# Performance work log

Measured on AMD Instinct MI355X. Metric: run time of the kernel, lower is better.

## Reference

```python
import jax, jax.numpy as jnp
import numpy as np

NUM_HEADS = 16
ROPE_BASE = 10000.0


def _rope_cos_sin(seq_len, head_dim, dtype):
    # freqs for the half-dim; original caches cat(freqs, freqs) and then applies
    # the rotation per-half, which is equivalent to using the half-size tables.
    inv_freq = 1.0 / (ROPE_BASE ** (jnp.arange(0, head_dim, 2, dtype=jnp.float32) / head_dim))
    t = jnp.arange(seq_len, dtype=jnp.float32)
    freqs = jnp.einsum('i,j->ij', t, inv_freq)  # [S, hd/2]
    return jnp.cos(freqs).astype(dtype), jnp.sin(freqs).astype(dtype)


def _apply_rotary(x, cos, sin):
    # x: [B, H, S, hd]; cos/sin: [S, hd/2] broadcast over B, H
    half = x.shape[-1] // 2
    x1, x2 = x[..., :half], x[..., half:]
    return jnp.concatenate([x1 * cos - x2 * sin, x2 * cos + x1 * sin], axis=-1)


def setup_inputs() -> dict:
    key = jax.random.key(0)
    ks = jax.random.split(key, 5)
    D = 2048
    B, S = 2, 2048
    std = 1.0 / np.sqrt(D)
    return {
        'x': jax.random.normal(ks[0], (B, S, D), dtype=jnp.float32),
        'Wq': jax.random.normal(ks[1], (D, D), dtype=jnp.float32) * std,
        'Wk': jax.random.normal(ks[2], (D, D), dtype=jnp.float32) * std,
        'Wv': jax.random.normal(ks[3], (D, D), dtype=jnp.float32) * std,
        'Wo': jax.random.normal(ks[4], (D, D), dtype=jnp.float32) * std,
    }


def reference(x, Wq, Wk, Wv, Wo):
    B, S, D = x.shape
    H = NUM_HEADS
    hd = D // H
    scale = hd ** -0.5

    def proj(W):  # torch Linear: y = x @ W.T -> [B, H, S, hd]
        return (x @ W.T).reshape(B, S, H, hd).transpose(0, 2, 1, 3)

    q, k, v = proj(Wq), proj(Wk), proj(Wv)

    cos, sin = _rope_cos_sin(S, hd, x.dtype)
    q = _apply_rotary(q, cos, sin)
    k = _apply_rotary(k, cos, sin)

    scores = jnp.einsum('bhqd,bhkd->bhqk', q, k) * scale  # full O(S^2) scores
    attn = jax.nn.softmax(scores, axis=-1)
    out = jnp.einsum('bhqk,bhkd->bhqd', attn, v)
    out = out.transpose(0, 2, 1, 3).reshape(B, S, D)
    return out @ Wo.T
```

## Files before the change

kernel.cpp:

```cpp
#include <hip/hip_runtime.h>
#include <cstdint>

typedef __attribute__((ext_vector_type(8))) short bf16x8;
typedef __attribute__((ext_vector_type(4))) float f32x4;
typedef __attribute__((ext_vector_type(16))) float f32x16;

__device__ inline unsigned short f2bf(float f) {
  uint32_t u = __float_as_uint(f);
  uint32_t lsb = (u >> 16) & 1u;
  u += 0x7fffu + lsb;
  return (unsigned short)(u >> 16);
}
__device__ inline float bf2f(unsigned short b) {
  return __uint_as_float(((uint32_t)b) << 16);
}
__device__ inline uint32_t cvt_pk_bf16(float lo, float hi) {
  uint32_t r;
  asm volatile("v_cvt_pk_bf16_f32 %0, %1, %2" : "=v"(r) : "v"(lo), "v"(hi));
  return r;
}

#define GLOAD16(gp, lp)                                                        \
  __builtin_amdgcn_global_load_lds(                                            \
      (const __attribute__((address_space(1))) void*)(gp),                     \
      (__attribute__((address_space(3))) void*)(lp), 16, 0, 0)

__global__ void cvt_f32_bf16(const float* __restrict__ in,
                             unsigned short* __restrict__ out, int n) {
  int i = (blockIdx.x * 256 + threadIdx.x) * 4;
  if (i >= n) return;
  float4 v = *(const float4*)(in + i);
  unsigned short o[4] = {f2bf(v.x), f2bf(v.y), f2bf(v.z), f2bf(v.w)};
  *(uint64_t*)(out + i) = *(const uint64_t*)o;
}

__global__ void rope_table_k(float* __restrict__ ctab, float* __restrict__ stab) {
  int i = blockIdx.x * 256 + threadIdx.x;
  int s = i >> 6, j = i & 63;
  float invf = expf(-(float)j * (9.210340371976184f / 64.0f));
  float ang = (float)s * invf;
  ctab[i] = cosf(ang);
  stab[i] = sinf(ang);
}

__global__ void rope_apply_k(unsigned short* __restrict__ qb,
                             unsigned short* __restrict__ kb,
                             const float* __restrict__ ctab,
                             const float* __restrict__ stab) {
  int row = blockIdx.x * 4 + (threadIdx.x >> 6);
  int t = threadIdx.x & 63;
  int s = row & 2047;
  int bh = (row >> 11) & 31;
  int isK = row >> 16;
  unsigned short* base = isK ? kb : qb;
  float qs = isK ? 1.0f : (0.08838834764831845f * 1.4426950408889634f);
  unsigned short* p = base + ((size_t)bh * 2048 + s) * 128;
  float c = ctab[s * 64 + t], sn = stab[s * 64 + t];
  float x1 = bf2f(p[t]), x2 = bf2f(p[t + 64]);
  p[t] = f2bf((x1 * c - x2 * sn) * qs);
  p[t + 64] = f2bf((x2 * c + x1 * sn) * qs);
}

__global__ void transpose_v_k(const unsigned short* __restrict__ v,
                              unsigned short* __restrict__ vt) {
  __shared__ unsigned short tile[64][72];
  int bh = blockIdx.x, st = blockIdx.y, dt = blockIdx.z;
  const unsigned short* src = v + ((size_t)bh * 2048 + st * 64) * 128 + dt * 64;
  unsigned short* dst = vt + ((size_t)bh * 128 + dt * 64) * 2048 + st * 64;
  int t = threadIdx.x;
  int r = t >> 2, c0 = (t & 3) * 16;
  *(bf16x8*)&tile[r][c0] = *(const bf16x8*)(src + (size_t)r * 128 + c0);
  *(bf16x8*)&tile[r][c0 + 8] = *(const bf16x8*)(src + (size_t)r * 128 + c0 + 8);
  __syncthreads();
  unsigned short o[16];
#pragma unroll
  for (int i = 0; i < 16; i++) o[i] = tile[c0 + i][r];
  *(bf16x8*)(dst + (size_t)r * 2048 + c0) = *(const bf16x8*)&o[0];
  *(bf16x8*)(dst + (size_t)r * 2048 + c0 + 8) = *(const bf16x8*)&o[8];
}

template <int EPI>
__global__ __launch_bounds__(256, 2) void gemm_bt(
    const unsigned short* __restrict__ A, const unsigned short* __restrict__ Bm,
    float* __restrict__ Cf, unsigned short* __restrict__ q_out,
    unsigned short* __restrict__ k_out, unsigned short* __restrict__ v_out,
    int M, int N, int K) {
  __shared__ unsigned short sA[128 * 32];
  __shared__ unsigned short sB[128 * 32];
  const int t = threadIdx.x;
  const int w = t >> 6, l = t & 63;
  const int wr = w >> 1, wc = w & 1;
  const int bm = blockIdx.x * 128, bn = blockIdx.y * 128;
  const int lr = l & 15, lg = l >> 4;
  f32x4 acc[4][4] = {};

  const int srow = w * 16 + (l >> 2);
  const int sseg = (l & 3) * 8;
  const unsigned short* ga = A + (size_t)(bm + srow) * K + sseg;
  const unsigned short* gb = Bm + (size_t)(bn + srow) * K + sseg;
  unsigned short* lA = sA + w * 512 + l * 8;
  unsigned short* lB = sB + w * 512 + l * 8;

  for (int kt = 0; kt < K; kt += 32) {
    __syncthreads();
    GLOAD16(ga + kt, lA);
    GLOAD16(ga + kt + (size_t)64 * K, lA + 2048);
    GLOAD16(gb + kt, lB);
    GLOAD16(gb + kt + (size_t)64 * K, lB + 2048);
    __syncthreads();
    bf16x8 af[4], bfv[4];
#pragma unroll
    for (int m = 0; m < 4; m++)
      af[m] = *(const bf16x8*)(sA + (wr * 64 + m * 16 + lr) * 32 + lg * 8);
#pragma unroll
    for (int n = 0; n < 4; n++)
      bfv[n] = *(const bf16x8*)(sB + (wc * 64 + n * 16 + lr) * 32 + lg * 8);
#pragma unroll
    for (int m = 0; m < 4; m++)
#pragma unroll
      for (int n = 0; n < 4; n++)
        acc[m][n] = __builtin_amdgcn_mfma_f32_16x16x32_bf16(af[m], bfv[n],
                                                            acc[m][n], 0, 0, 0);
  }

#pragma unroll
  for (int m = 0; m < 4; m++) {
#pragma unroll
    for (int n = 0; n < 4; n++) {
      int gm0 = bm + wr * 64 + m * 16 + lg * 4;
      int gn = bn + wc * 64 + n * 16 + lr;
#pragma unroll
      for (int j = 0; j < 4; j++) {
        float v = acc[m][n][j];
        int gm = gm0 + j;
        if (EPI == 0) {
          Cf[(size_t)gm * N + gn] = v;
        } else {
          int which = gn >> 11, rem = gn & 2047;
          int h = rem >> 7, d = rem & 127;
          int b = gm >> 11, s = gm & 2047;
          unsigned short* dst = which == 0 ? q_out : (which == 1 ? k_out : v_out);
          dst[(((size_t)(b * 16 + h)) * 2048 + s) * 128 + d] = f2bf(v);
        }
      }
    }
  }
}

template <int EPI>
__global__ __launch_bounds__(512, 1) void gemm256(
    const unsigned short* __restrict__ A, const unsigned short* __restrict__ Bm,
    float* __restrict__ Cf, unsigned short* __restrict__ q_out,
    unsigned short* __restrict__ k_out, unsigned short* __restrict__ v_out,
    int M, int N, int K, int nbm) {
  __shared__ unsigned short sA[2][2][256 * 32];
  __shared__ unsigned short sB[2][2][256 * 32];

  const int t = threadIdx.x;
  const int w = t >> 6, l = t & 63;
  const int wr = w >> 2, wc = w & 3;
  const int lr = l & 15, lg = l >> 4;
  const int gsw = (lg ^ (lr & 3)) * 8;

  const int cpx = gridDim.x >> 3;
  const int bid = blockIdx.x;
  const int swz = (bid & 7) * cpx + (bid >> 3);
  const int bm = (swz % nbm) * 256, bn = (swz / nbm) * 256;

  f32x4 acc[8][4] = {};

  int rowi[2], goff[2];
#pragma unroll
  for (int i = 0; i < 2; i++) {
    int idx = i * 512 + t;
    rowi[i] = idx >> 2;
    goff[i] = ((idx & 3) ^ (rowi[i] & 3)) * 8;
  }
  const unsigned short* Ab = A + (size_t)bm * K;
  const unsigned short* Bb = Bm + (size_t)bn * K;

#define STAGE256(Xb, plane, koff)                                              \
  do {                                                                         \
    _Pragma("unroll") for (int i = 0; i < 2; i++)                              \
        GLOAD16(Xb + (size_t)rowi[i] * K + (koff) + goff[i],                   \
                (plane) + (i * 512 + t) * 8);                                  \
  } while (0)

  STAGE256(Ab, sA[0][0], 0);
  STAGE256(Bb, sB[0][0], 0);
  STAGE256(Ab, sA[0][1], 32);
  STAGE256(Bb, sB[0][1], 32);
  asm volatile("s_waitcnt vmcnt(4)" ::: "memory");
  __builtin_amdgcn_s_barrier();

  const int NT = K >> 6;
  for (int t2 = 0; t2 < NT; ++t2) {
    const int db = t2 & 1, dn = db ^ 1;
    const int kt = (t2 + 1 < NT ? t2 + 1 : t2) * 64;
    bf16x8 a[4], a2[4], b[4];

#pragma unroll
    for (int mf = 0; mf < 4; mf++)
      a[mf] = *(const bf16x8*)&sA[db][0][(wr * 128 + mf * 16 + lr) * 32 + gsw];
#pragma unroll
    for (int nf = 0; nf < 4; nf++)
      b[nf] = *(const bf16x8*)&sB[db][0][(wc * 64 + nf * 16 + lr) * 32 + gsw];
    STAGE256(Ab, sA[dn][0], kt);
    __builtin_amdgcn_s_barrier();
    asm volatile("s_waitcnt lgkmcnt(0)" ::: "memory");
    __builtin_amdgcn_sched_barrier(0);
    __builtin_amdgcn_s_setprio(1);
#pragma unroll
    for (int mf = 0; mf < 4; mf++)
#pragma unroll
      for (int nf = 0; nf < 4; nf++)
        acc[mf][nf] = __builtin_amdgcn_mfma_f32_16x16x32_bf16(a[mf], b[nf],
                                                              acc[mf][nf], 0, 0, 0);
    __builtin_amdgcn_s_setprio(0);
    __builtin_amdgcn_s_barrier();

#pragma unroll
    for (int mf = 0; mf < 4; mf++)
      a2[mf] = *(const bf16x8*)&sA[db][0][(wr * 128 + (mf + 4) * 16 + lr) * 32 + gsw];
    STAGE256(Bb, sB[dn][0], kt);
    __builtin_amdgcn_s_barrier();
    asm volatile("s_waitcnt lgkmcnt(0)" ::: "memory");
    __builtin_amdgcn_sched_barrier(0);
    __builtin_amdgcn_s_setprio(1);
#pragma unroll
    for (int mf = 0; mf < 4; mf++)
#pragma unroll
      for (int nf = 0; nf < 4; nf++)
        acc[mf + 4][nf] = __builtin_amdgcn_mfma_f32_16x16x32_bf16(
            a2[mf], b[nf], acc[mf + 4][nf], 0, 0, 0);
    __builtin_amdgcn_s_setprio(0);
    asm volatile("s_waitcnt vmcnt(4)" ::: "memory");
    __builtin_amdgcn_s_barrier();

#pragma unroll
    for (int mf = 0; mf < 4; mf++)
      a[mf] = *(const bf16x8*)&sA[db][1][(wr * 128 + mf * 16 + lr) * 32 + gsw];
#pragma unroll
    for (int nf = 0; nf < 4; nf++)
      b[nf] = *(const bf16x8*)&sB[db][1][(wc * 64 + nf * 16 + lr) * 32 + gsw];
    STAGE256(Ab, sA[dn][1], kt + 32);
    __builtin_amdgcn_s_barrier();
    asm volatile("s_waitcnt lgkmcnt(0)" ::: "memory");
    __builtin_amdgcn_sched_barrier(0);
    __builtin_amdgcn_s_setprio(1);
#pragma unroll
    for (int mf = 0; mf < 4; mf++)
#pragma unroll
      for (int nf = 0; nf < 4; nf++)
        acc[mf][nf] = __builtin_amdgcn_mfma_f32_16x16x32_bf16(a[mf], b[nf],
                                                              acc[mf][nf], 0, 0, 0);
    __builtin_amdgcn_s_setprio(0);
    __builtin_amdgcn_s_barrier();

#pragma unroll
    for (int mf = 0; mf < 4; mf++)
      a2[mf] = *(const bf16x8*)&sA[db][1][(wr * 128 + (mf + 4) * 16 + lr) * 32 + gsw];
    STAGE256(Bb, sB[dn][1], kt + 32);
    __builtin_amdgcn_s_barrier();
    asm volatile("s_waitcnt lgkmcnt(0)" ::: "memory");
    __builtin_amdgcn_sched_barrier(0);
    __builtin_amdgcn_s_setprio(1);
#pragma unroll
    for (int mf = 0; mf < 4; mf++)
#pragma unroll
      for (int nf = 0; nf < 4; nf++)
        acc[mf + 4][nf] = __builtin_amdgcn_mfma_f32_16x16x32_bf16(
            a2[mf], b[nf], acc[mf + 4][nf], 0, 0, 0);
    __builtin_amdgcn_s_setprio(0);
    asm volatile("s_waitcnt vmcnt(4)" ::: "memory");
    __builtin_amdgcn_s_barrier();
  }

#pragma unroll
  for (int mf = 0; mf < 8; mf++) {
#pragma unroll
    for (int nf = 0; nf < 4; nf++) {
      int gm0 = bm + wr * 128 + mf * 16 + lg * 4;
      int gn = bn + wc * 64 + nf * 16 + lr;
#pragma unroll
      for (int j = 0; j < 4; j++) {
        float v = acc[mf][nf][j];
        int gm = gm0 + j;
        if (EPI == 0) {
          Cf[(size_t)gm * N + gn] = v;
        } else {
          int which = gn >> 11, rem = gn & 2047;
          int h = rem >> 7, d = rem & 127;
          int b = gm >> 11, s = gm & 2047;
          unsigned short* dst = which == 0 ? q_out : (which == 1 ? k_out : v_out);
          dst[(((size_t)(b * 16 + h)) * 2048 + s) * 128 + d] = f2bf(v);
        }
      }
    }
  }
}

__global__ __launch_bounds__(256, 2) void attn_k(
    const unsigned short* __restrict__ Q, const unsigned short* __restrict__ K,
    const unsigned short* __restrict__ Vt, unsigned short* __restrict__ ctx) {
  __shared__ unsigned short sK[2][64 * 128];
  __shared__ unsigned short sV[2][128 * 64];

  const int qt = blockIdx.x, bh = blockIdx.y;
  const int t = threadIdx.x;
  const int w = t >> 6, l = t & 63;
  const int lq = l & 31;
  const int h5 = l >> 5;
  const int b = bh >> 4, hh = bh & 15;
  const int q0 = qt * 128 + w * 32;
  const unsigned short* Qp = Q + ((size_t)bh * 2048 + q0) * 128;
  const unsigned short* Kbh = K + (size_t)bh * 2048 * 128;
  const unsigned short* Vbh = Vt + (size_t)bh * 128 * 2048;

  int gko[4], gvo[4];
#pragma unroll
  for (int i = 0; i < 4; i++) {
    int p = i * 256 + t;
    int rK = p >> 4, cK = p & 15;
    gko[i] = rK * 128 + ((cK ^ (rK & 7)) * 8);
    int rV = p >> 3, cV = p & 7;
    gvo[i] = rV * 2048 + ((cV ^ (rV & 7)) * 8);
  }

  bf16x8 qf[8];
#pragma unroll
  for (int st = 0; st < 8; st++)
    qf[st] = *(const bf16x8*)(Qp + lq * 128 + st * 16 + h5 * 8);

  f32x16 o[4];
#pragma unroll
  for (int db = 0; db < 4; db++) o[db] = (f32x16)0.0f;
  float m_r = -1e30f, l_r = 0.0f;

#define STAGE_KV(buf, kv)                                                      \
  do {                                                                         \
    _Pragma("unroll") for (int i = 0; i < 4; i++)                              \
        GLOAD16(Kbh + (size_t)(kv)*128 + gko[i],                               \
                sK[buf] + (i * 256 + t) * 8);                                  \
    _Pragma("unroll") for (int i = 0; i < 4; i++)                              \
        GLOAD16(Vbh + (size_t)(kv) + gvo[i], sV[buf] + (i * 256 + t) * 8);     \
  } while (0)

  STAGE_KV(0, 0);
  __syncthreads();

  for (int it = 0; it < 32; ++it) {
    const int cur = it & 1;
    if (it < 31) STAGE_KV(cur ^ 1, (it + 1) * 64);

    const char* kbuf = (const char*)sK[cur];
    const char* vbuf = (const char*)sV[cur];

    f32x16 s2[2];
#pragma unroll
    for (int kb2 = 0; kb2 < 2; kb2++) {
      s2[kb2] = (f32x16)0.0f;
      const int rr = kb2 * 32 + lq;
      const int swzz = (rr & 7) << 4;
#pragma unroll
      for (int st = 0; st < 8; st++) {
        bf16x8 kf = *(const bf16x8*)(kbuf + rr * 256 + ((st * 32 + h5 * 16) ^ swzz));
        s2[kb2] = __builtin_amdgcn_mfma_f32_32x32x16_bf16(kf, qf[st], s2[kb2], 0, 0, 0);
      }
    }

    float sm[32];
#pragma unroll
    for (int kb2 = 0; kb2 < 2; kb2++)
#pragma unroll
      for (int r = 0; r < 16; r++) sm[kb2 * 16 + r] = s2[kb2][r];

    float tmax = sm[0];
#pragma unroll
    for (int i = 1; i < 32; i++) tmax = fmaxf(tmax, sm[i]);
    tmax = fmaxf(tmax, __shfl_xor(tmax, 32));

    if (!__all(tmax <= m_r + 8.0f)) {
      float m_new = fmaxf(m_r, tmax);
      float fac = exp2f(m_r - m_new);
      l_r *= fac;
      float fo[16];
#pragma unroll
      for (int r = 0; r < 16; r++)
        fo[r] = __shfl(fac, (r & 3) + 8 * (r >> 2) + 4 * h5);
#pragma unroll
      for (int db = 0; db < 4; db++)
#pragma unroll
        for (int r = 0; r < 16; r++) o[db][r] *= fo[r];
      m_r = m_new;
    }

    float psum = 0.0f;
#pragma unroll
    for (int i = 0; i < 32; i++) {
      sm[i] = exp2f(sm[i] - m_r);
      psum += sm[i];
    }
    psum += __shfl_xor(psum, 32);
    l_r += psum;

    uint32_t wAp[2][4], wBp[2][4];
#pragma unroll
    for (int kb2 = 0; kb2 < 2; kb2++)
#pragma unroll
      for (int rq = 0; rq < 4; rq++) {
        wAp[kb2][rq] = cvt_pk_bf16(sm[kb2 * 16 + rq * 4 + 0], sm[kb2 * 16 + rq * 4 + 1]);
        wBp[kb2][rq] = cvt_pk_bf16(sm[kb2 * 16 + rq * 4 + 2], sm[kb2 * 16 + rq * 4 + 3]);
      }

#pragma unroll
    for (int st = 0; st < 4; st++) {
      const int kb2 = st >> 1, p2 = (st & 1) * 2;
      uint32_t keepA = h5 ? wAp[kb2][p2 + 1] : wAp[kb2][p2];
      uint32_t keepB = h5 ? wBp[kb2][p2 + 1] : wBp[kb2][p2];
      uint32_t sendA = h5 ? wAp[kb2][p2] : wAp[kb2][p2 + 1];
      uint32_t sendB = h5 ? wBp[kb2][p2] : wBp[kb2][p2 + 1];
      uint32_t partA = __shfl_xor(sendA, 32);
      uint32_t partB = __shfl_xor(sendB, 32);
      union {
        uint32_t u[4];
        bf16x8 v;
      } pu;
      pu.u[0] = h5 ? partA : keepA;
      pu.u[1] = h5 ? partB : keepB;
      pu.u[2] = h5 ? keepA : partA;
      pu.u[3] = h5 ? keepB : partB;
#pragma unroll
      for (int db = 0; db < 4; db++) {
        const int rv = db * 32 + lq;
        const int swzz = (rv & 7) << 4;
        bf16x8 vb = *(const bf16x8*)(vbuf + rv * 128 + ((st * 32 + h5 * 16) ^ swzz));
        o[db] = __builtin_amdgcn_mfma_f32_32x32x16_bf16(pu.v, vb, o[db], 0, 0, 0);
      }
    }
    __syncthreads();
  }

  float inv = 1.0f / l_r;
  float io[16];
#pragma unroll
  for (int r = 0; r < 16; r++)
    io[r] = __shfl(inv, (r & 3) + 8 * (r >> 2) + 4 * h5);
#pragma unroll
  for (int db = 0; db < 4; db++) {
#pragma unroll
    for (int r = 0; r < 16; r++) {
      int s = q0 + (r & 3) + 8 * (r >> 2) + 4 * h5;
      ctx[((size_t)(b * 2048 + s)) * 2048 + hh * 128 + db * 32 + lq] =
          f2bf(o[db][r] * io[r]);
    }
  }
}

extern "C" void kernel_launch(void* const* d_in, const int* in_sizes, int n_in,
                              void* d_out, int out_size, void* d_ws,
                              size_t ws_size, hipStream_t stream) {
  const float* x = (const float*)d_in[0];
  const float* Wq = (const float*)d_in[1];
  const float* Wk = (const float*)d_in[2];
  const float* Wv = (const float*)d_in[3];
  const float* Wo = (const float*)d_in[4];
  float* out = (float*)d_out;

  const size_t BS = 4096;
  const size_t D = 2048;

  char* p = (char*)d_ws;
  unsigned short* xb = (unsigned short*)p;   p += BS * D * 2;
  unsigned short* wqkv = (unsigned short*)p; p += 3 * D * D * 2;
  unsigned short* wo = (unsigned short*)p;   p += D * D * 2;
  unsigned short* qb = (unsigned short*)p;   p += BS * D * 2;
  unsigned short* kb = (unsigned short*)p;   p += BS * D * 2;
  unsigned short* vb = (unsigned short*)p;   p += BS * D * 2;
  float* ctab = (float*)p;                   p += 2048 * 64 * 4;
  float* stab = (float*)p;                   p += 2048 * 64 * 4;
  unsigned short* vt = wqkv;
  unsigned short* ctx = xb;

  cvt_f32_bf16<<<8388608 / 1024, 256, 0, stream>>>(x, xb, 8388608);
  cvt_f32_bf16<<<4194304 / 1024, 256, 0, stream>>>(Wq, wqkv, 4194304);
  cvt_f32_bf16<<<4194304 / 1024, 256, 0, stream>>>(Wk, wqkv + 4194304, 4194304);
  cvt_f32_bf16<<<4194304 / 1024, 256, 0, stream>>>(Wv, wqkv + 8388608, 4194304);
  cvt_f32_bf16<<<4194304 / 1024, 256, 0, stream>>>(Wo, wo, 4194304);
  rope_table_k<<<131072 / 256, 256, 0, stream>>>(ctab, stab);

  gemm256<1><<<384, 512, 0, stream>>>(xb, wqkv, nullptr, qb, kb, vb, 4096, 6144,
                                      2048, 16);
  rope_apply_k<<<32768, 256, 0, stream>>>(qb, kb, ctab, stab);
  transpose_v_k<<<dim3(32, 32, 2), 256, 0, stream>>>(vb, vt);
  attn_k<<<dim3(16, 32), 256, 0, stream>>>(qb, kb, vt, ctx);
  gemm_bt<0><<<dim3(32, 16), 256, 0, stream>>>(ctx, wo, out, nullptr, nullptr,
                                               nullptr, 4096, 2048, 2048);
}
```

Baseline: 355.6 us.

## Retile QKV projection GEMM to 256x192 tiles for full CU coverage

Changes the fused QKV GEMM tile from 256x256 to 256x192, raising the grid from 384 to 512 blocks so all CUs of the device get one block each (M=4096/256=16, N=6144/192=32). The B tile is now staged with both K-halves in a single 3-load pass, and the vmcnt waits are adjusted to match. The LDS swizzle changes to XOR on (row>>1)&3. The cost is a smaller per-block tile with lower arithmetic intensity and a reworked wait schedule that could stall or race if the counts are off.

```diff
diff --git a/kernel.cpp b/kernel.cpp
--- a/kernel.cpp
+++ b/kernel.cpp
@@ -154,58 +154,66 @@
     unsigned short* __restrict__ k_out, unsigned short* __restrict__ v_out,
     int M, int N, int K, int nbm) {
   __shared__ unsigned short sA[2][2][256 * 32];
-  __shared__ unsigned short sB[2][2][256 * 32];
+  __shared__ unsigned short sB[2][2][192 * 32];
 
   const int t = threadIdx.x;
   const int w = t >> 6, l = t & 63;
   const int wr = w >> 2, wc = w & 3;
   const int lr = l & 15, lg = l >> 4;
-  const int gsw = (lg ^ (lr & 3)) * 8;
+  const int gsw = (lg ^ ((lr >> 1) & 3)) * 8;
 
   const int cpx = gridDim.x >> 3;
   const int bid = blockIdx.x;
   const int swz = (bid & 7) * cpx + (bid >> 3);
-  const int bm = (swz % nbm) * 256, bn = (swz / nbm) * 256;
-
-  f32x4 acc[8][4] = {};
-
-  int rowi[2], goff[2];
-#pragma unroll
-  for (int i = 0; i < 2; i++) {
-    int idx = i * 512 + t;
-    rowi[i] = idx >> 2;
-    goff[i] = ((idx & 3) ^ (rowi[i] & 3)) * 8;
-  }
+  const int bm = (swz % nbm) * 256, bn = (swz / nbm) * 192;
+
+  f32x4 acc[8][3] = {};
+
   const unsigned short* Ab = A + (size_t)bm * K;
   const unsigned short* Bb = Bm + (size_t)bn * K;
 
-#define STAGE256(Xb, plane, koff)                                              \
+#define STAGE_A(plane, koff)                                                   \
   do {                                                                         \
-    _Pragma("unroll") for (int i = 0; i < 2; i++)                              \
-        GLOAD16(Xb + (size_t)rowi[i] * K + (koff) + goff[i],                   \
-                (plane) + (i * 512 + t) * 8);                                  \
+    _Pragma("unroll") for (int i = 0; i < 2; i++) {                            \
+      int g = i * 512 + t;                                                     \
+      int row = g >> 2, c = g & 3;                                             \
+      GLOAD16(Ab + (size_t)row * K + (koff) + ((c ^ ((row >> 1) & 3)) * 8),    \
+              (plane) + g * 8);                                                \
+    }                                                                          \
   } while (0)
 
-  STAGE256(Ab, sA[0][0], 0);
-  STAGE256(Bb, sB[0][0], 0);
-  STAGE256(Ab, sA[0][1], 32);
-  STAGE256(Bb, sB[0][1], 32);
-  asm volatile("s_waitcnt vmcnt(4)" ::: "memory");
+#define STAGE_B(plane, koff)                                                   \
+  do {                                                                         \
+    _Pragma("unroll") for (int i = 0; i < 3; i++) {                            \
+      int g = i * 512 + t;                                                     \
+      int kh = (g >= 768) ? 1 : 0;                                             \
+      int gr = g - kh * 768;                                                   \
+      int row = gr >> 2, c = gr & 3;                                           \
+      GLOAD16(Bb + (size_t)row * K + (koff) + kh * 32 +                        \
+                  ((c ^ ((row >> 1) & 3)) * 8),                                \
+              (plane) + g * 8);                                                \
+    }                                                                          \
+  } while (0)
+
+  STAGE_B(&sB[0][0][0], 0);
+  STAGE_A(&sA[0][0][0], 0);
+  STAGE_A(&sA[0][1][0], 32);
+  asm volatile("s_waitcnt vmcnt(2)" ::: "memory");
   __builtin_amdgcn_s_barrier();
 
   const int NT = K >> 6;
   for (int t2 = 0; t2 < NT; ++t2) {
     const int db = t2 & 1, dn = db ^ 1;
     const int kt = (t2 + 1 < NT ? t2 + 1 : t2) * 64;
-    bf16x8 a[4], a2[4], b[4];
+    bf16x8 a[4], a2[4], b[3];
 
 #pragma unroll
     for (int mf = 0; mf < 4; mf++)
       a[mf] = *(const bf16x8*)&sA[db][0][(wr * 128 + mf * 16 + lr) * 32 + gsw];
 #pragma unroll
-    for (int nf = 0; nf < 4; nf++)
-      b[nf] = *(const bf16x8*)&sB[db][0][(wc * 64 + nf * 16 + lr) * 32 + gsw];
-    STAGE256(Ab, sA[dn][0], kt);
+    for (int nf = 0; nf < 3; nf++)
+      b[nf] = *(const bf16x8*)&sB[db][0][(wc * 48 + nf * 16 + lr) * 32 + gsw];
+    STAGE_B(&sB[dn][0][0], kt);
     __builtin_amdgcn_s_barrier();
     asm volatile("s_waitcnt lgkmcnt(0)" ::: "memory");
     __builtin_amdgcn_sched_barrier(0);
@@ -213,7 +221,7 @@
 #pragma unroll
     for (int mf = 0; mf < 4; mf++)
 #pragma unroll
-      for (int nf = 0; nf < 4; nf++)
+      for (int nf = 0; nf < 3; nf++)
         acc[mf][nf] = __builtin_amdgcn_mfma_f32_16x16x32_bf16(a[mf], b[nf],
                                                               acc[mf][nf], 0, 0, 0);
     __builtin_amdgcn_s_setprio(0);
@@ -222,7 +230,7 @@
 #pragma unroll
     for (int mf = 0; mf < 4; mf++)
       a2[mf] = *(const bf16x8*)&sA[db][0][(wr * 128 + (mf + 4) * 16 + lr) * 32 + gsw];
-    STAGE256(Bb, sB[dn][0], kt);
+    STAGE_A(&sA[dn][0][0], kt);
     __builtin_amdgcn_s_barrier();
     asm volatile("s_waitcnt lgkmcnt(0)" ::: "memory");
     __builtin_amdgcn_sched_barrier(0);
@@ -230,20 +238,20 @@
 #pragma unroll
     for (int mf = 0; mf < 4; mf++)
 #pragma unroll
-      for (int nf = 0; nf < 4; nf++)
+      for (int nf = 0; nf < 3; nf++)
         acc[mf + 4][nf] = __builtin_amdgcn_mfma_f32_16x16x32_bf16(
             a2[mf], b[nf], acc[mf + 4][nf], 0, 0, 0);
     __builtin_amdgcn_s_setprio(0);
-    asm volatile("s_waitcnt vmcnt(4)" ::: "memory");
+    asm volatile("s_waitcnt vmcnt(5)" ::: "memory");
     __builtin_amdgcn_s_barrier();
 
 #pragma unroll
     for (int mf = 0; mf < 4; mf++)
       a[mf] = *(const bf16x8*)&sA[db][1][(wr * 128 + mf * 16 + lr) * 32 + gsw];
 #pragma unroll
-    for (int nf = 0; nf < 4; nf++)
-      b[nf] = *(const bf16x8*)&sB[db][1][(wc * 64 + nf * 16 + lr) * 32 + gsw];
-    STAGE256(Ab, sA[dn][1], kt + 32);
+    for (int nf = 0; nf < 3; nf++)
+      b[nf] = *(const bf16x8*)&sB[db][1][(wc * 48 + nf * 16 + lr) * 32 + gsw];
+    STAGE_A(&sA[dn][1][0], kt + 32);
     __builtin_amdgcn_s_barrier();
     asm volatile("s_waitcnt lgkmcnt(0)" ::: "memory");
     __builtin_amdgcn_sched_barrier(0);
@@ -251,7 +259,7 @@
 #pragma unroll
     for (int mf = 0; mf < 4; mf++)
 #pragma unroll
-      for (int nf = 0; nf < 4; nf++)
+      for (int nf = 0; nf < 3; nf++)
         acc[mf][nf] = __builtin_amdgcn_mfma_f32_16x16x32_bf16(a[mf], b[nf],
                                                               acc[mf][nf], 0, 0, 0);
     __builtin_amdgcn_s_setprio(0);
@@ -260,7 +268,6 @@
 #pragma unroll
     for (int mf = 0; mf < 4; mf++)
       a2[mf] = *(const bf16x8*)&sA[db][1][(wr * 128 + (mf + 4) * 16 + lr) * 32 + gsw];
-    STAGE256(Bb, sB[dn][1], kt + 32);
     __builtin_amdgcn_s_barrier();
     asm volatile("s_waitcnt lgkmcnt(0)" ::: "memory");
     __builtin_amdgcn_sched_barrier(0);
@@ -268,20 +275,20 @@
 #pragma unroll
     for (int mf = 0; mf < 4; mf++)
 #pragma unroll
-      for (int nf = 0; nf < 4; nf++)
+      for (int nf = 0; nf < 3; nf++)
         acc[mf + 4][nf] = __builtin_amdgcn_mfma_f32_16x16x32_bf16(
             a2[mf], b[nf], acc[mf + 4][nf], 0, 0, 0);
     __builtin_amdgcn_s_setprio(0);
-    asm volatile("s_waitcnt vmcnt(4)" ::: "memory");
+    asm volatile("s_waitcnt vmcnt(2)" ::: "memory");
     __builtin_amdgcn_s_barrier();
   }
 
 #pragma unroll
   for (int mf = 0; mf < 8; mf++) {
 #pragma unroll
-    for (int nf = 0; nf < 4; nf++) {
+    for (int nf = 0; nf < 3; nf++) {
       int gm0 = bm + wr * 128 + mf * 16 + lg * 4;
-      int gn = bn + wc * 64 + nf * 16 + lr;
+      int gn = bn + wc * 48 + nf * 16 + lr;
 #pragma unroll
       for (int j = 0; j < 4; j++) {
         float v = acc[mf][nf][j];
@@ -489,7 +496,7 @@
   cvt_f32_bf16<<<4194304 / 1024, 256, 0, stream>>>(Wo, wo, 4194304);
   rope_table_k<<<131072 / 256, 256, 0, stream>>>(ctab, stab);
 
-  gemm256<1><<<384, 512, 0, stream>>>(xb, wqkv, nullptr, qb, kb, vb, 4096, 6144,
+  gemm256<1><<<512, 512, 0, stream>>>(xb, wqkv, nullptr, qb, kb, vb, 4096, 6144,
                                       2048, 16);
   rope_apply_k<<<32768, 256, 0, stream>>>(qb, kb, ctab, stab);
   transpose_v_k<<<dim3(32, 32, 2), 256, 0, stream>>>(vb, vt);
```

Result: faster. 301.5 us (-15.2%).
